# Kernel tuning notes

Hardware: AMD Instinct MI355X
Metric: run time of the kernel (lower is better)

Reference implementation:

```python
import jax, jax.numpy as jnp
import numpy as np
from jax import lax

TAU = 0.25
N_TIMESTEPS = 12
OUTPUT_TICKS = 4
INPUT_DIM = 1024
HIDDEN = 1024
OUTPUT_DIM = 1024
CLEANUP = 512
BATCH = 1024
W_SD = 0.1


def setup_inputs() -> dict:
    key = jax.random.key(0)
    ks = jax.random.split(key, 6)
    inputs = jax.random.normal(ks[0], (BATCH, N_TIMESTEPS, INPUT_DIM), dtype=jnp.float32)
    w_oh = W_SD * jax.random.normal(ks[1], (INPUT_DIM, HIDDEN), dtype=jnp.float32)
    w_hp = W_SD * jax.random.normal(ks[2], (HIDDEN, OUTPUT_DIM), dtype=jnp.float32)
    w_pp = W_SD * jax.random.normal(ks[3], (OUTPUT_DIM, OUTPUT_DIM), dtype=jnp.float32)
    w_pc = W_SD * jax.random.normal(ks[4], (OUTPUT_DIM, CLEANUP), dtype=jnp.float32)
    w_cp = W_SD * jax.random.normal(ks[5], (CLEANUP, OUTPUT_DIM), dtype=jnp.float32)
    bias_h = jnp.zeros((HIDDEN,), jnp.float32)
    bias_p = jnp.zeros((OUTPUT_DIM,), jnp.float32)
    bias_c = jnp.zeros((CLEANUP,), jnp.float32)
    return {"inputs": inputs, "w_oh": w_oh, "w_hp": w_hp, "w_pp": w_pp,
            "w_pc": w_pc, "w_cp": w_cp, "bias_h": bias_h, "bias_p": bias_p,
            "bias_c": bias_c}


def reference(inputs, w_oh, w_hp, w_pp, w_pc, w_cp, bias_h, bias_p, bias_c):
    B = inputs.shape[0]
    act = jax.nn.sigmoid
    # time-major input stream: step t consumes o_input[:, t-1, :]
    x = jnp.swapaxes(inputs, 0, 1)  # [T, B, I]

    in_h0 = jnp.zeros((B, HIDDEN), jnp.float32)
    in_p0 = jnp.zeros((B, OUTPUT_DIM), jnp.float32)
    in_c0 = jnp.zeros((B, CLEANUP), jnp.float32)
    carry0 = (in_h0, in_p0, in_c0, in_h0 + 0.5, in_p0 + 0.5, in_c0 + 0.5)

    def step(carry, o_t):
        in_h, in_p, in_c, a_h, a_p, a_c = carry
        # leaky-integrator blends; hp/pp/cp/pc all use PREVIOUS step activations
        h = TAU * (o_t @ w_oh + bias_h) + (1.0 - TAU) * in_h
        p = TAU * (a_h @ w_hp + a_p @ w_pp + a_c @ w_cp + bias_p) + (1.0 - TAU) * in_p
        c = TAU * (a_p @ w_pc + bias_c) + (1.0 - TAU) * in_c
        a_p_new = act(p)
        new_carry = (h, p, c, act(h), a_p_new, act(c))
        return new_carry, a_p_new

    _, act_p_seq = lax.scan(step, carry0, x)  # [T, B, OUTPUT_DIM]
    return act_p_seq[-OUTPUT_TICKS:]  # [OUTPUT_TICKS, B, OUTPUT_DIM]
```

## Files before the change

### kernel.cpp

```cpp
#include <hip/hip_runtime.h>
#include <cstdint>
#include <cstddef>


typedef _Float16 half8 __attribute__((ext_vector_type(8)));
typedef float floatx4 __attribute__((ext_vector_type(4)));

__device__ __forceinline__ void async_cp16(const void* g, void* l) {
  __builtin_amdgcn_global_load_lds(
      (const __attribute__((address_space(1))) void*)g,
      (__attribute__((address_space(3))) void*)l, 16, 0, 0);
}

__device__ __forceinline__ float sigmoidf_(float x) {
  return 1.f / (1.f + __expf(-x));
}

__global__ __launch_bounds__(256) void k_transpose(
    const float* __restrict__ src, int K, int N,
    _Float16* __restrict__ dst, int dst_ld, int k_off) {
  __shared__ float tile[64][65];
  const int k0 = blockIdx.y * 64, n0 = blockIdx.x * 64;
  const int tx = threadIdx.x & 63, ty = threadIdx.x >> 6;
#pragma unroll
  for (int j = 0; j < 16; ++j) {
    int kr = j * 4 + ty;
    tile[kr][tx] = src[(size_t)(k0 + kr) * N + n0 + tx];
  }
  __syncthreads();
#pragma unroll
  for (int j = 0; j < 16; ++j) {
    int nr = j * 4 + ty;
    dst[(size_t)(n0 + nr) * dst_ld + k_off + k0 + tx] = (_Float16)tile[tx][nr];
  }
}

__global__ __launch_bounds__(256) void k_pack_frag(
    const float* __restrict__ src, int N, _Float16* __restrict__ dst,
    int kStride, int kOffChunks) {
  __shared__ float tile[64][65];
  const int k0 = blockIdx.y * 64, n0 = blockIdx.x * 64;
  const int tx = threadIdx.x & 63, ty = threadIdx.x >> 6;
#pragma unroll
  for (int jj = 0; jj < 16; ++jj) {
    int kr = jj * 4 + ty;
    tile[kr][tx] = src[(size_t)(k0 + kr) * N + n0 + tx];
  }
  __syncthreads();
  const int j = threadIdx.x >> 6, lane = threadIdx.x & 63;
  const int r16 = lane & 15, quad = lane >> 4;
#pragma unroll
  for (int c = 0; c < 2; ++c) {
    half8 v;
#pragma unroll
    for (int u = 0; u < 8; ++u)
      v[u] = (_Float16)tile[c * 32 + quad * 8 + u][j * 16 + r16];
    const int kcG = kOffChunks + blockIdx.y * 2 + c;
    *(half8*)(dst + ((size_t)(blockIdx.x * kStride + kcG) * 4 + j) * 512 +
              lane * 8) = v;
  }
}

__global__ __launch_bounds__(256) void k_prep(
    const float* __restrict__ x, _Float16* __restrict__ U,
    _Float16* __restrict__ AH0, _Float16* __restrict__ AP0,
    _Float16* __restrict__ AC0, float* __restrict__ Pst,
    float* __restrict__ Cst) {
  const int id = blockIdx.x * 256 + threadIdx.x;
  const int b = id >> 10, i = id & 1023;
  const float* xb = x + (size_t)b * 12 * 1024 + i;
  float g = 0.f;
#pragma unroll
  for (int t = 0; t < 11; ++t) {
    g = xb[t * 1024] + 0.75f * g;
    U[(size_t)t * 1048576 + id] = (_Float16)g;
  }
  AH0[id] = (_Float16)0.5f;
  AP0[id] = (_Float16)0.5f;
  Pst[id] = 0.f;
  if (i < 512) {
    const int cid = b * 512 + i;
    AC0[cid] = (_Float16)0.5f;
    Cst[cid] = 0.f;
  }
}

__global__ __launch_bounds__(64) void k_gemm_big(
    const _Float16* __restrict__ A, const _Float16* __restrict__ B,
    const float* __restrict__ bias, _Float16* __restrict__ dst, int mode) {
  __shared__ __align__(16) _Float16 sA[2 * 4096];
  __shared__ __align__(16) _Float16 sB[2 * 4096];
  const int lane = threadIdx.x;
  const int mBase = blockIdx.y * 64, nBase = blockIdx.x * 64;
  const int r16 = lane & 15, quad = lane >> 4, mrow = lane >> 3;
  const int gsw = ((lane & 7) ^ (mrow & 7)) * 8;
  const floatx4 zero = {0.f, 0.f, 0.f, 0.f};
  floatx4 acc[4][4];
#pragma unroll
  for (int i = 0; i < 4; ++i)
#pragma unroll
    for (int j = 0; j < 4; ++j) acc[i][j] = zero;

  const _Float16* Abase = A + (size_t)(mBase + mrow) * 1024 + gsw;
  const _Float16* Bbase = B + (size_t)(nBase + mrow) * 1024 + gsw;

  auto stage = [&](int kt, int buf) {
    const int k0 = kt << 6;
#pragma unroll
    for (int q = 0; q < 8; ++q)
      async_cp16(Abase + (size_t)q * 8192 + k0, sA + buf * 4096 + q * 512);
#pragma unroll
    for (int q = 0; q < 8; ++q)
      async_cp16(Bbase + (size_t)q * 8192 + k0, sB + buf * 4096 + q * 512);
  };

  stage(0, 0);
  for (int kt = 0; kt < 16; ++kt) {
    if (kt + 1 < 16) {
      stage(kt + 1, (kt + 1) & 1);
      asm volatile("s_waitcnt vmcnt(16)" ::: "memory");
    } else {
      asm volatile("s_waitcnt vmcnt(0)" ::: "memory");
    }
    const _Float16* sa = sA + (kt & 1) * 4096;
    const _Float16* sb = sB + (kt & 1) * 4096;
#pragma unroll
    for (int kk = 0; kk < 2; ++kk) {
      const int sw = ((kk * 4 + quad) ^ (r16 & 7)) * 8;
      half8 af[4], bf[4];
#pragma unroll
      for (int i = 0; i < 4; ++i) af[i] = *(const half8*)&sa[(i * 16 + r16) * 64 + sw];
#pragma unroll
      for (int j = 0; j < 4; ++j) bf[j] = *(const half8*)&sb[(j * 16 + r16) * 64 + sw];
#pragma unroll
      for (int i = 0; i < 4; ++i)
#pragma unroll
        for (int j = 0; j < 4; ++j)
          acc[i][j] =
              __builtin_amdgcn_mfma_f32_16x16x32_f16(af[i], bf[j], acc[i][j], 0, 0, 0);
    }
  }

  if (mode == 0) {
    const int tm1 = mBase >> 10;
    const float beta = 1.f - __powf(0.75f, (float)(tm1 + 1));
    _Float16* o = dst + (size_t)(mBase + 1024) * 1024;
#pragma unroll
    for (int i = 0; i < 4; ++i)
#pragma unroll
      for (int j = 0; j < 4; ++j) {
        const int n = nBase + j * 16 + r16;
#pragma unroll
        for (int r = 0; r < 4; ++r) {
          const int row = i * 16 + quad * 4 + r;
          const float h = 0.25f * acc[i][j][r] + beta * bias[n];
          o[(size_t)row * 1024 + n] = (_Float16)sigmoidf_(h);
        }
      }
  } else {
    _Float16* o = dst + (size_t)mBase * 1024;
#pragma unroll
    for (int i = 0; i < 4; ++i)
#pragma unroll
      for (int j = 0; j < 4; ++j) {
        const int n = nBase + j * 16 + r16;
#pragma unroll
        for (int r = 0; r < 4; ++r) {
          const int row = i * 16 + quad * 4 + r;
          o[(size_t)row * 1024 + n] = (_Float16)(0.25f * (acc[i][j][r] + bias[n]));
        }
      }
  }
}

__global__ __launch_bounds__(256, 3) void k_step(
    const _Float16* __restrict__ Qt, const _Float16* __restrict__ APc,
    const _Float16* __restrict__ ACc, _Float16* __restrict__ APn,
    _Float16* __restrict__ ACn, const _Float16* __restrict__ Wrf,
    const _Float16* __restrict__ Wcf, const float* __restrict__ bias_c,
    float* __restrict__ Pst, float* __restrict__ Cst,
    float* __restrict__ out_t) {
  __shared__ float red[4][2][4][4][64];
  const int lane = threadIdx.x & 63, w = threadIdx.x >> 6;
  const int r16 = lane & 15, quad = lane >> 4;
  const int blk = blockIdx.x;
  const bool isP = blk < 512;
  int mBase, nt;
  if (isP) {
    mBase = (blk >> 4) * 32;
    nt = blk & 15;
  } else {
    const int b = blk - 512;
    mBase = (b >> 3) * 32;
    nt = b & 7;
  }
  const int nBase = nt * 64;
  const floatx4 zero = {0.f, 0.f, 0.f, 0.f};
  floatx4 acc[2][4];
#pragma unroll
  for (int i = 0; i < 2; ++i)
#pragma unroll
    for (int j = 0; j < 4; ++j) acc[i][j] = zero;

  half8 abuf[3][2], bbuf[3][4];
  auto MM = [&](half8* af, half8* bf) {
#pragma unroll
    for (int i = 0; i < 2; ++i)
#pragma unroll
      for (int j = 0; j < 4; ++j)
        acc[i][j] = __builtin_amdgcn_mfma_f32_16x16x32_f16(af[i], bf[j],
                                                           acc[i][j], 0, 0, 0);
  };

  if (isP) {
    const int kcBase = w * 12;
    auto LD = [&](half8* af, half8* bf, int c) {
      const int kc = kcBase + c;
      const int kg = kc * 32;
      if (kc < 32) {
#pragma unroll
        for (int i = 0; i < 2; ++i)
          af[i] = *(const half8*)(APc + (size_t)(mBase + i * 16 + r16) * 1024 +
                                  kg + quad * 8);
      } else {
#pragma unroll
        for (int i = 0; i < 2; ++i)
          af[i] = *(const half8*)(ACc + (size_t)(mBase + i * 16 + r16) * 512 +
                                  (kg - 1024) + quad * 8);
      }
      const _Float16* wp = Wrf + (size_t)(nt * 48 + kc) * 2048 + lane * 8;
#pragma unroll
      for (int j = 0; j < 4; ++j) bf[j] = *(const half8*)(wp + j * 512);
    };
    LD(abuf[0], bbuf[0], 0);
    LD(abuf[1], bbuf[1], 1);
#pragma unroll
    for (int c = 0; c < 12; ++c) {
      if (c + 2 < 12) LD(abuf[(c + 2) % 3], bbuf[(c + 2) % 3], c + 2);
      MM(abuf[c % 3], bbuf[c % 3]);
    }
  } else {
    const int kcBase = w * 8;
    auto LD = [&](half8* af, half8* bf, int c) {
      const int kc = kcBase + c;
      const int kg = kc * 32;
#pragma unroll
      for (int i = 0; i < 2; ++i)
        af[i] = *(const half8*)(APc + (size_t)(mBase + i * 16 + r16) * 1024 +
                                kg + quad * 8);
      const _Float16* wp = Wcf + (size_t)(nt * 32 + kc) * 2048 + lane * 8;
#pragma unroll
      for (int j = 0; j < 4; ++j) bf[j] = *(const half8*)(wp + j * 512);
    };
    LD(abuf[0], bbuf[0], 0);
    LD(abuf[1], bbuf[1], 1);
#pragma unroll
    for (int c = 0; c < 8; ++c) {
      if (c + 2 < 8) LD(abuf[(c + 2) % 3], bbuf[(c + 2) % 3], c + 2);
      MM(abuf[c % 3], bbuf[c % 3]);
    }
  }

#pragma unroll
  for (int i = 0; i < 2; ++i)
#pragma unroll
    for (int j = 0; j < 4; ++j)
#pragma unroll
      for (int r = 0; r < 4; ++r) red[w][i][j][r][lane] = acc[i][j][r];
  __syncthreads();

  if (isP) {
#pragma unroll
    for (int i = 0; i < 2; ++i) {
      const int n = nBase + w * 16 + r16;
#pragma unroll
      for (int r = 0; r < 4; ++r) {
        const float v = red[0][i][w][r][lane] + red[1][i][w][r][lane] +
                        red[2][i][w][r][lane] + red[3][i][w][r][lane];
        const int b = mBase + i * 16 + quad * 4 + r;
        const size_t o = (size_t)b * 1024 + n;
        const float pn = 0.25f * v + (float)Qt[o] + 0.75f * Pst[o];
        Pst[o] = pn;
        const float a = sigmoidf_(pn);
        APn[o] = (_Float16)a;
        if (out_t) out_t[o] = a;
      }
    }
  } else {
#pragma unroll
    for (int i = 0; i < 2; ++i) {
      const int n = nBase + w * 16 + r16;
#pragma unroll
      for (int r = 0; r < 4; ++r) {
        const float v = red[0][i][w][r][lane] + red[1][i][w][r][lane] +
                        red[2][i][w][r][lane] + red[3][i][w][r][lane];
        const int b = mBase + i * 16 + quad * 4 + r;
        const size_t o = (size_t)b * 512 + n;
        const float cn = 0.25f * (v + bias_c[n]) + 0.75f * Cst[o];
        Cst[o] = cn;
        ACn[o] = (_Float16)sigmoidf_(cn);
      }
    }
  }
}

extern "C" void kernel_launch(void* const* d_in, const int* in_sizes, int n_in,
                              void* d_out, int out_size, void* d_ws,
                              size_t ws_size, hipStream_t stream) {
  const float* x      = (const float*)d_in[0];
  const float* w_oh   = (const float*)d_in[1];
  const float* w_hp   = (const float*)d_in[2];
  const float* w_pp   = (const float*)d_in[3];
  const float* w_pc   = (const float*)d_in[4];
  const float* w_cp   = (const float*)d_in[5];
  const float* bias_h = (const float*)d_in[6];
  const float* bias_p = (const float*)d_in[7];
  const float* bias_c = (const float*)d_in[8];
  float* out = (float*)d_out;

  uint8_t* p = (uint8_t*)d_ws;
  _Float16* Wrf  = (_Float16*)p; p += (size_t)1024 * 1536 * 2;
  _Float16* Wcf  = (_Float16*)p; p += (size_t)512 * 1024 * 2;
  _Float16* WohT = (_Float16*)p; p += (size_t)1024 * 1024 * 2;
  _Float16* Whp  = (_Float16*)p; p += (size_t)1024 * 1024 * 2;
  _Float16* U    = (_Float16*)p; p += (size_t)11 * 1048576 * 2;
  _Float16* AH   = (_Float16*)p; p += (size_t)12 * 1048576 * 2;
  _Float16* Q    = (_Float16*)p; p += (size_t)12 * 1048576 * 2;
  _Float16* AP0  = (_Float16*)p; p += (size_t)1048576 * 2;
  _Float16* AP1  = (_Float16*)p; p += (size_t)1048576 * 2;
  _Float16* AC0  = (_Float16*)p; p += (size_t)512 * 1024 * 2;
  _Float16* AC1  = (_Float16*)p; p += (size_t)512 * 1024 * 2;
  float* Pst = (float*)p; p += (size_t)1048576 * 4;
  float* Cst = (float*)p; p += (size_t)512 * 1024 * 4;

  const dim3 blk256(256);
  k_transpose<<<dim3(16, 16), blk256, 0, stream>>>(w_oh, 1024, 1024, WohT, 1024, 0);
  k_transpose<<<dim3(16, 16), blk256, 0, stream>>>(w_hp, 1024, 1024, Whp, 1024, 0);
  k_pack_frag<<<dim3(16, 16), blk256, 0, stream>>>(w_pp, 1024, Wrf, 48, 0);
  k_pack_frag<<<dim3(16, 8),  blk256, 0, stream>>>(w_cp, 1024, Wrf, 48, 32);
  k_pack_frag<<<dim3(8, 16),  blk256, 0, stream>>>(w_pc, 512, Wcf, 32, 0);
  k_prep<<<4096, blk256, 0, stream>>>(x, U, AH, AP0, AC0, Pst, Cst);
  k_gemm_big<<<dim3(16, 176), dim3(64), 0, stream>>>(U, WohT, bias_h, AH, 0);
  k_gemm_big<<<dim3(16, 192), dim3(64), 0, stream>>>(AH, Whp, bias_p, Q, 1);
  for (int t = 0; t < 12; ++t) {
    const _Float16* APc = (t & 1) ? AP1 : AP0;
    _Float16* APn       = (t & 1) ? AP0 : AP1;
    const _Float16* ACc = (t & 1) ? AC1 : AC0;
    _Float16* ACn       = (t & 1) ? AC0 : AC1;
    float* ot = (t >= 8) ? out + (size_t)(t - 8) * 1048576 : (float*)nullptr;
    k_step<<<dim3(768), blk256, 0, stream>>>(Q + (size_t)t * 1048576, APc,
                                             ACc, APn, ACn, Wrf, Wcf, bias_c,
                                             Pst, Cst, ot);
  }
}
```

Before: 435.1 us.

## Merge prep launches, retile big GEMM to 128x128, special-case first Q step

Merges the two transpose launches and the three fragment-pack launches into single kernels indexed by grid z. Replaces the t=0 hidden-to-output GEMM with a column-sum kernel, since the initial hidden activation is the constant 0.5. Retiles the large GEMM to 256-thread 128x128 blocks where each wave loads a quarter of the tiles, dropping the double-buffered async pipeline for a single buffer with barriers. Also remaps step-kernel block indices and deepens the register prefetch from 3 to 4 stages. The GEMM loses load/compute overlap, and k_q0 is a serial, badly parallelised kernel with only four blocks.

```diff
diff --git a/kernel.cpp b/kernel.cpp
--- a/kernel.cpp
+++ b/kernel.cpp
@@ -16,28 +16,44 @@
   return 1.f / (1.f + __expf(-x));
 }
 
-__global__ __launch_bounds__(256) void k_transpose(
-    const float* __restrict__ src, int K, int N,
-    _Float16* __restrict__ dst, int dst_ld, int k_off) {
+__global__ __launch_bounds__(256) void k_trans_all(
+    const float* __restrict__ w_oh, const float* __restrict__ w_hp,
+    _Float16* __restrict__ WohT, _Float16* __restrict__ Whp) {
+  const float* src = blockIdx.z ? w_hp : w_oh;
+  _Float16* dst = blockIdx.z ? Whp : WohT;
   __shared__ float tile[64][65];
   const int k0 = blockIdx.y * 64, n0 = blockIdx.x * 64;
   const int tx = threadIdx.x & 63, ty = threadIdx.x >> 6;
 #pragma unroll
   for (int j = 0; j < 16; ++j) {
     int kr = j * 4 + ty;
-    tile[kr][tx] = src[(size_t)(k0 + kr) * N + n0 + tx];
+    tile[kr][tx] = src[(size_t)(k0 + kr) * 1024 + n0 + tx];
   }
   __syncthreads();
 #pragma unroll
   for (int j = 0; j < 16; ++j) {
     int nr = j * 4 + ty;
-    dst[(size_t)(n0 + nr) * dst_ld + k_off + k0 + tx] = (_Float16)tile[tx][nr];
-  }
-}
-
-__global__ __launch_bounds__(256) void k_pack_frag(
-    const float* __restrict__ src, int N, _Float16* __restrict__ dst,
-    int kStride, int kOffChunks) {
+    dst[(size_t)(n0 + nr) * 1024 + k0 + tx] = (_Float16)tile[tx][nr];
+  }
+}
+
+__global__ __launch_bounds__(256) void k_pack_all(
+    const float* __restrict__ w_pp, const float* __restrict__ w_cp,
+    const float* __restrict__ w_pc, _Float16* __restrict__ Wrf,
+    _Float16* __restrict__ Wcf) {
+  const int z = blockIdx.z;
+  const float* src;
+  _Float16* dst;
+  int N, kStride, kOff;
+  if (z == 0) {
+    src = w_pp; dst = Wrf; N = 1024; kStride = 48; kOff = 0;
+  } else if (z == 1) {
+    if (blockIdx.y >= 8) return;
+    src = w_cp; dst = Wrf; N = 1024; kStride = 48; kOff = 32;
+  } else {
+    if (blockIdx.x >= 8) return;
+    src = w_pc; dst = Wcf; N = 512; kStride = 32; kOff = 0;
+  }
   __shared__ float tile[64][65];
   const int k0 = blockIdx.y * 64, n0 = blockIdx.x * 64;
   const int tx = threadIdx.x & 63, ty = threadIdx.x >> 6;
@@ -55,17 +71,26 @@
 #pragma unroll
     for (int u = 0; u < 8; ++u)
       v[u] = (_Float16)tile[c * 32 + quad * 8 + u][j * 16 + r16];
-    const int kcG = kOffChunks + blockIdx.y * 2 + c;
+    const int kcG = kOff + blockIdx.y * 2 + c;
     *(half8*)(dst + ((size_t)(blockIdx.x * kStride + kcG) * 4 + j) * 512 +
               lane * 8) = v;
   }
 }
 
+__global__ __launch_bounds__(256) void k_q0(
+    const float* __restrict__ w_hp, const float* __restrict__ bias_p,
+    _Float16* __restrict__ Q) {
+  const int n = blockIdx.x * 256 + threadIdx.x;
+  float s = 0.f;
+  for (int k = 0; k < 1024; ++k) s += w_hp[(size_t)k * 1024 + n];
+  const _Float16 q = (_Float16)(0.25f * (0.5f * s + bias_p[n]));
+  for (int b = 0; b < 1024; ++b) Q[(size_t)b * 1024 + n] = q;
+}
+
 __global__ __launch_bounds__(256) void k_prep(
     const float* __restrict__ x, _Float16* __restrict__ U,
-    _Float16* __restrict__ AH0, _Float16* __restrict__ AP0,
-    _Float16* __restrict__ AC0, float* __restrict__ Pst,
-    float* __restrict__ Cst) {
+    _Float16* __restrict__ AP0, _Float16* __restrict__ AC0,
+    float* __restrict__ Pst, float* __restrict__ Cst) {
   const int id = blockIdx.x * 256 + threadIdx.x;
   const int b = id >> 10, i = id & 1023;
   const float* xb = x + (size_t)b * 12 * 1024 + i;
@@ -75,7 +100,6 @@
     g = xb[t * 1024] + 0.75f * g;
     U[(size_t)t * 1048576 + id] = (_Float16)g;
   }
-  AH0[id] = (_Float16)0.5f;
   AP0[id] = (_Float16)0.5f;
   Pst[id] = 0.f;
   if (i < 512) {
@@ -85,13 +109,13 @@
   }
 }
 
-__global__ __launch_bounds__(64) void k_gemm_big(
+__global__ __launch_bounds__(256) void k_gemm_big(
     const _Float16* __restrict__ A, const _Float16* __restrict__ B,
     const float* __restrict__ bias, _Float16* __restrict__ dst, int mode) {
-  __shared__ __align__(16) _Float16 sA[2 * 4096];
-  __shared__ __align__(16) _Float16 sB[2 * 4096];
-  const int lane = threadIdx.x;
-  const int mBase = blockIdx.y * 64, nBase = blockIdx.x * 64;
+  __shared__ __align__(16) _Float16 sA[8192];
+  __shared__ __align__(16) _Float16 sB[8192];
+  const int lane = threadIdx.x & 63, w = threadIdx.x >> 6;
+  const int mBase = blockIdx.y * 128, nBase = blockIdx.x * 128;
   const int r16 = lane & 15, quad = lane >> 4, mrow = lane >> 3;
   const int gsw = ((lane & 7) ^ (mrow & 7)) * 8;
   const floatx4 zero = {0.f, 0.f, 0.f, 0.f};
@@ -101,37 +125,30 @@
 #pragma unroll
     for (int j = 0; j < 4; ++j) acc[i][j] = zero;
 
-  const _Float16* Abase = A + (size_t)(mBase + mrow) * 1024 + gsw;
-  const _Float16* Bbase = B + (size_t)(nBase + mrow) * 1024 + gsw;
-
-  auto stage = [&](int kt, int buf) {
+  const _Float16* gbase =
+      (w < 2 ? A + (size_t)(mBase + (w & 1) * 64 + mrow) * 1024
+             : B + (size_t)(nBase + (w & 1) * 64 + mrow) * 1024) +
+      gsw;
+  _Float16* lbase = (w < 2 ? sA : sB) + (w & 1) * 4096;
+  const int wi = w >> 1, wj = w & 1;
+  const _Float16* csa = sA + wi * 4096;
+  const _Float16* csb = sB + wj * 4096;
+
+  for (int kt = 0; kt < 16; ++kt) {
     const int k0 = kt << 6;
 #pragma unroll
     for (int q = 0; q < 8; ++q)
-      async_cp16(Abase + (size_t)q * 8192 + k0, sA + buf * 4096 + q * 512);
-#pragma unroll
-    for (int q = 0; q < 8; ++q)
-      async_cp16(Bbase + (size_t)q * 8192 + k0, sB + buf * 4096 + q * 512);
-  };
-
-  stage(0, 0);
-  for (int kt = 0; kt < 16; ++kt) {
-    if (kt + 1 < 16) {
-      stage(kt + 1, (kt + 1) & 1);
-      asm volatile("s_waitcnt vmcnt(16)" ::: "memory");
-    } else {
-      asm volatile("s_waitcnt vmcnt(0)" ::: "memory");
-    }
-    const _Float16* sa = sA + (kt & 1) * 4096;
-    const _Float16* sb = sB + (kt & 1) * 4096;
+      async_cp16(gbase + (size_t)q * 8192 + k0, lbase + q * 512);
+    asm volatile("s_waitcnt vmcnt(0)" ::: "memory");
+    __syncthreads();
 #pragma unroll
     for (int kk = 0; kk < 2; ++kk) {
       const int sw = ((kk * 4 + quad) ^ (r16 & 7)) * 8;
       half8 af[4], bf[4];
 #pragma unroll
-      for (int i = 0; i < 4; ++i) af[i] = *(const half8*)&sa[(i * 16 + r16) * 64 + sw];
-#pragma unroll
-      for (int j = 0; j < 4; ++j) bf[j] = *(const half8*)&sb[(j * 16 + r16) * 64 + sw];
+      for (int i = 0; i < 4; ++i) af[i] = *(const half8*)&csa[(i * 16 + r16) * 64 + sw];
+#pragma unroll
+      for (int j = 0; j < 4; ++j) bf[j] = *(const half8*)&csb[(j * 16 + r16) * 64 + sw];
 #pragma unroll
       for (int i = 0; i < 4; ++i)
 #pragma unroll
@@ -139,17 +156,20 @@
           acc[i][j] =
               __builtin_amdgcn_mfma_f32_16x16x32_f16(af[i], bf[j], acc[i][j], 0, 0, 0);
     }
-  }
-
+    __syncthreads();
+  }
+
+  const int rowQ = mBase + wi * 64;
+  const int colQ = nBase + wj * 64;
   if (mode == 0) {
     const int tm1 = mBase >> 10;
     const float beta = 1.f - __powf(0.75f, (float)(tm1 + 1));
-    _Float16* o = dst + (size_t)(mBase + 1024) * 1024;
+    _Float16* o = dst + (size_t)(rowQ + 1024) * 1024;
 #pragma unroll
     for (int i = 0; i < 4; ++i)
 #pragma unroll
       for (int j = 0; j < 4; ++j) {
-        const int n = nBase + j * 16 + r16;
+        const int n = colQ + j * 16 + r16;
 #pragma unroll
         for (int r = 0; r < 4; ++r) {
           const int row = i * 16 + quad * 4 + r;
@@ -158,12 +178,12 @@
         }
       }
   } else {
-    _Float16* o = dst + (size_t)mBase * 1024;
+    _Float16* o = dst + (size_t)rowQ * 1024;
 #pragma unroll
     for (int i = 0; i < 4; ++i)
 #pragma unroll
       for (int j = 0; j < 4; ++j) {
-        const int n = nBase + j * 16 + r16;
+        const int n = colQ + j * 16 + r16;
 #pragma unroll
         for (int r = 0; r < 4; ++r) {
           const int row = i * 16 + quad * 4 + r;
@@ -187,12 +207,12 @@
   const bool isP = blk < 512;
   int mBase, nt;
   if (isP) {
-    mBase = (blk >> 4) * 32;
-    nt = blk & 15;
+    nt = (blk & 7) | ((blk & 256) ? 8 : 0);
+    mBase = ((blk >> 3) & 31) * 32;
   } else {
     const int b = blk - 512;
+    nt = b & 7;
     mBase = (b >> 3) * 32;
-    nt = b & 7;
   }
   const int nBase = nt * 64;
   const floatx4 zero = {0.f, 0.f, 0.f, 0.f};
@@ -202,7 +222,7 @@
 #pragma unroll
     for (int j = 0; j < 4; ++j) acc[i][j] = zero;
 
-  half8 abuf[3][2], bbuf[3][4];
+  half8 abuf[4][2], bbuf[4][4];
   auto MM = [&](half8* af, half8* bf) {
 #pragma unroll
     for (int i = 0; i < 2; ++i)
@@ -234,10 +254,11 @@
     };
     LD(abuf[0], bbuf[0], 0);
     LD(abuf[1], bbuf[1], 1);
+    LD(abuf[2], bbuf[2], 2);
 #pragma unroll
     for (int c = 0; c < 12; ++c) {
-      if (c + 2 < 12) LD(abuf[(c + 2) % 3], bbuf[(c + 2) % 3], c + 2);
-      MM(abuf[c % 3], bbuf[c % 3]);
+      if (c + 3 < 12) LD(abuf[(c + 3) & 3], bbuf[(c + 3) & 3], c + 3);
+      MM(abuf[c & 3], bbuf[c & 3]);
     }
   } else {
     const int kcBase = w * 8;
@@ -254,10 +275,11 @@
     };
     LD(abuf[0], bbuf[0], 0);
     LD(abuf[1], bbuf[1], 1);
+    LD(abuf[2], bbuf[2], 2);
 #pragma unroll
     for (int c = 0; c < 8; ++c) {
-      if (c + 2 < 8) LD(abuf[(c + 2) % 3], bbuf[(c + 2) % 3], c + 2);
-      MM(abuf[c % 3], bbuf[c % 3]);
+      if (c + 3 < 8) LD(abuf[(c + 3) & 3], bbuf[(c + 3) & 3], c + 3);
+      MM(abuf[c & 3], bbuf[c & 3]);
     }
   }
 
@@ -334,14 +356,13 @@
   float* Cst = (float*)p; p += (size_t)512 * 1024 * 4;
 
   const dim3 blk256(256);
-  k_transpose<<<dim3(16, 16), blk256, 0, stream>>>(w_oh, 1024, 1024, WohT, 1024, 0);
-  k_transpose<<<dim3(16, 16), blk256, 0, stream>>>(w_hp, 1024, 1024, Whp, 1024, 0);
-  k_pack_frag<<<dim3(16, 16), blk256, 0, stream>>>(w_pp, 1024, Wrf, 48, 0);
-  k_pack_frag<<<dim3(16, 8),  blk256, 0, stream>>>(w_cp, 1024, Wrf, 48, 32);
-  k_pack_frag<<<dim3(8, 16),  blk256, 0, stream>>>(w_pc, 512, Wcf, 32, 0);
-  k_prep<<<4096, blk256, 0, stream>>>(x, U, AH, AP0, AC0, Pst, Cst);
-  k_gemm_big<<<dim3(16, 176), dim3(64), 0, stream>>>(U, WohT, bias_h, AH, 0);
-  k_gemm_big<<<dim3(16, 192), dim3(64), 0, stream>>>(AH, Whp, bias_p, Q, 1);
+  k_trans_all<<<dim3(16, 16, 2), blk256, 0, stream>>>(w_oh, w_hp, WohT, Whp);
+  k_pack_all<<<dim3(16, 16, 3), blk256, 0, stream>>>(w_pp, w_cp, w_pc, Wrf, Wcf);
+  k_q0<<<dim3(4), blk256, 0, stream>>>(w_hp, bias_p, Q);
+  k_prep<<<4096, blk256, 0, stream>>>(x, U, AP0, AC0, Pst, Cst);
+  k_gemm_big<<<dim3(8, 88), blk256, 0, stream>>>(U, WohT, bias_h, AH, 0);
+  k_gemm_big<<<dim3(8, 88), blk256, 0, stream>>>(AH + 1048576, Whp, bias_p,
+                                                 Q + 1048576, 1);
   for (int t = 0; t < 12; ++t) {
     const _Float16* APc = (t & 1) ? AP1 : AP0;
     _Float16* APn       = (t & 1) ? AP0 : AP1;
```

New measurement: 465.8 us. 1.07x slower.
